# Kernel optimization log

Measured on AMD Instinct MI355X. Metric: run time of the kernel, lower is better.

The kernel has to match this reference:

```python
import jax, jax.numpy as jnp
import numpy as np
from jax import lax

B, V, ENC = 64, 2048, 128   # batch, total_voxels, encoder_dim
T = 100                      # max caption length
EMB, DEC, ATT, VOCAB = 256, 512, 256, 29


def setup_inputs() -> dict:
    key = jax.random.key(0)
    ks = jax.random.split(key, 24)
    u = lambda k, shape, s=0.1: jax.random.uniform(k, shape, jnp.float32, -s, s)
    inp = {}
    inp['encoder_output'] = jax.random.normal(ks[0], (B, V, ENC), jnp.float32)
    inp['captions'] = jax.random.randint(ks[1], (B, T), 0, VOCAB)
    # lengths sorted descending (torch loop assumes this); max length == T
    lens = jnp.sort(jax.random.randint(ks[2], (B,), 1, T + 1))[::-1]
    inp['caption_lengths'] = lens.at[0].set(T)
    # parameters (torch Linear: y = x @ W.T + b; kaiming-ish uniform)
    inp['emb_W'] = u(ks[3], (VOCAB, EMB))                       # embed init uniform(-0.1,0.1)
    inp['W_enc'] = u(ks[4], (ATT, ENC), ENC ** -0.5)
    inp['b_enc'] = u(ks[5], (ATT,), ENC ** -0.5)
    inp['W_dec'] = u(ks[6], (ATT, DEC), DEC ** -0.5)
    inp['b_dec'] = u(ks[7], (ATT,), DEC ** -0.5)
    inp['w_full'] = u(ks[8], (ATT,), ATT ** -0.5)               # full_att weight [1,ATT] -> vector
    inp['b_full'] = u(ks[9], (), ATT ** -0.5)
    lstm_in = EMB + ENC
    inp['W_ih'] = u(ks[10], (4 * DEC, lstm_in), DEC ** -0.5)
    inp['b_ih'] = u(ks[11], (4 * DEC,), DEC ** -0.5)
    inp['W_hh'] = u(ks[12], (4 * DEC, DEC), DEC ** -0.5)
    inp['b_hh'] = u(ks[13], (4 * DEC,), DEC ** -0.5)
    inp['W_init_h'] = u(ks[14], (DEC, ENC), ENC ** -0.5)
    inp['b_init_h'] = u(ks[15], (DEC,), ENC ** -0.5)
    inp['W_init_c'] = u(ks[16], (DEC, ENC), ENC ** -0.5)
    inp['b_init_c'] = u(ks[17], (DEC,), ENC ** -0.5)
    inp['W_beta'] = u(ks[18], (ENC, DEC), DEC ** -0.5)
    inp['b_beta'] = u(ks[19], (ENC,), DEC ** -0.5)
    inp['W_final'] = u(ks[20], (VOCAB, DEC))                    # uniform(-0.1,0.1) per init_weights
    inp['b_final'] = jnp.zeros((VOCAB,), jnp.float32)
    return inp


def reference(encoder_output, captions, caption_lengths, emb_W,
              W_enc, b_enc, W_dec, b_dec, w_full, b_full,
              W_ih, b_ih, W_hh, b_hh,
              W_init_h, b_init_h, W_init_c, b_init_c,
              W_beta, b_beta, W_final, b_final):
    # dropout in eval mode (identity) for deterministic reference
    emb = emb_W[captions]                                  # [B,T,EMB]
    enc_att = encoder_output @ W_enc.T + b_enc             # [B,V,ATT] (loop-invariant)
    mean_enc = encoder_output.mean(axis=1)                 # [B,ENC]
    h0 = mean_enc @ W_init_h.T + b_init_h                  # [B,DEC]
    c0 = mean_enc @ W_init_c.T + b_init_c
    lengths = caption_lengths

    def step(carry, xs):
        h, c = carry
        emb_t, t = xs                                      # [B,EMB], scalar
        # additive attention
        dec_att = h @ W_dec.T + b_dec                      # [B,ATT]
        scores = jax.nn.relu(enc_att + dec_att[:, None, :]) @ w_full + b_full  # [B,V]
        alpha = jax.nn.softmax(scores, axis=1)
        awe = jnp.einsum('bv,bve->be', alpha, encoder_output)                   # [B,ENC]
        gate = jax.nn.sigmoid(h @ W_beta.T + b_beta)
        awe = gate * awe
        # LSTMCell (torch gate order: i, f, g, o)
        x = jnp.concatenate([emb_t, awe], axis=1)          # [B,EMB+ENC]
        gates = x @ W_ih.T + b_ih + h @ W_hh.T + b_hh      # [B,4*DEC]
        i, f, g, o = jnp.split(gates, 4, axis=1)
        i, f, o = jax.nn.sigmoid(i), jax.nn.sigmoid(f), jax.nn.sigmoid(o)
        g = jnp.tanh(g)
        c_new = f * c + i * g
        h_new = o * jnp.tanh(c_new)
        pred = h_new @ W_final.T + b_final                 # [B,VOCAB]
        # length-based truncation: only rows with t < length are updated
        m = (t < lengths)[:, None]
        h2 = jnp.where(m, h_new, h)
        c2 = jnp.where(m, c_new, c)
        pred = jnp.where(m, pred, 0.0)
        alpha = jnp.where(m, alpha, 0.0)
        return (h2, c2), (pred, alpha)

    (_, _), (preds, alphas) = lax.scan(
        step, (h0, c0), (emb.transpose(1, 0, 2), jnp.arange(T)))
    predictions = preds.transpose(1, 0, 2)                 # [B,T,VOCAB]
    alphas = alphas.transpose(1, 0, 2)                     # [B,T,V]
    return predictions, alphas, caption_lengths
```

## Files before the change

kernel.cpp:

```cpp
#include <hip/hip_runtime.h>
#include <hip/hip_bf16.h>

#define BB 64
#define VV 2048
#define ENCD 128
#define TT 100
#define EMBD 256
#define DECD 512
#define ATTD 256
#define NVOCAB 29

typedef unsigned int u32;
typedef unsigned short u16;
typedef __attribute__((ext_vector_type(2))) float f2;

__device__ __forceinline__ float sigf(float x) { return 1.0f / (1.0f + __expf(-x)); }
__device__ __forceinline__ u16 to_bf16(float f) {
    u32 u = __float_as_uint(f);
    u += 0x7fffu + ((u >> 16) & 1u);
    return (u16)(u >> 16);
}

#if __has_builtin(__builtin_amdgcn_cvt_pk_fp8_f32) && __has_builtin(__builtin_amdgcn_cvt_pk_f32_fp8)
#define HAVE_FP8_CVT 1
#endif

__device__ __forceinline__ u32 fp8_enc(float f) {
#ifdef HAVE_FP8_CVT
    return (u32)__builtin_amdgcn_cvt_pk_fp8_f32(f, f, 0, false) & 0xffu;
#else
    u32 u = __float_as_uint(f);
    u32 s = (u >> 24) & 0x80u;
    u32 a = u & 0x7fffffffu;
    u32 r = a + 0x7FFFFu + ((a >> 20) & 1u);
    int v = (int)(r >> 20) - (120 << 3);
    if (v < 8) v = 0;
    if (v > 0x7E) v = 0x7E;
    return s | (u32)v;
#endif
}
__device__ __forceinline__ void fp8x4_dec(u32 u, float* o) {
#ifdef HAVE_FP8_CVT
    f2 lo = __builtin_amdgcn_cvt_pk_f32_fp8((int)u, false);
    f2 hi = __builtin_amdgcn_cvt_pk_f32_fp8((int)u, true);
    o[0] = lo[0]; o[1] = lo[1]; o[2] = hi[0]; o[3] = hi[1];
#else
    #pragma unroll
    for (int i = 0; i < 4; i++) {
        u32 byte = (u >> (8 * i)) & 0xffu;
        u32 s = (byte & 0x80u) << 24;
        u32 m = byte & 0x7fu;
        o[i] = m ? __uint_as_float(s | ((m + (120u << 3)) << 20)) : __uint_as_float(s);
    }
#endif
}


__global__ __launch_bounds__(256) void k_transpose(const float* __restrict__ W_dec,
                                                   const float* __restrict__ W_beta,
                                                   const float* __restrict__ W_ih,
                                                   const float* __restrict__ W_enc,
                                                   float* __restrict__ W_decT,
                                                   float* __restrict__ W_betaT,
                                                   float* __restrict__ W2T,
                                                   float* __restrict__ W_encT) {
    int i = blockIdx.x * 256 + threadIdx.x;
    if (i < DECD * ATTD) {
        int l = i / ATTD, a = i % ATTD;
        W_decT[i] = W_dec[a * DECD + l];
    } else if (i < DECD * ATTD + DECD * ENCD) {
        int j = i - DECD * ATTD;
        int l = j / ENCD, e = j % ENCD;
        W_betaT[j] = W_beta[e * DECD + l];
    } else if (i < DECD * ATTD + DECD * ENCD + ENCD * 2048) {
        int j = i - (DECD * ATTD + DECD * ENCD);
        int e = j >> 11, g = j & 2047;
        W2T[j] = W_ih[g * 384 + 256 + e];
    } else if (i < DECD * ATTD + DECD * ENCD + ENCD * 2048 + ENCD * ATTD) {
        int j = i - (DECD * ATTD + DECD * ENCD + ENCD * 2048);
        int k = j / ATTD, a = j % ATTD;
        W_encT[j] = W_enc[a * ENCD + k];
    }
}

__global__ __launch_bounds__(256) void k_enc_att(const float* __restrict__ enc,
                                                 const float* __restrict__ W_encT,
                                                 const float* __restrict__ b_enc,
                                                 unsigned char* __restrict__ enc_att8,
                                                 u16* __restrict__ enc_bf) {
    __shared__ float tile[64][ENCD + 1];
    int b = blockIdx.y, v0 = blockIdx.x * 64;
    int t = threadIdx.x;
    const float* src = enc + ((size_t)b * VV + v0) * ENCD;
    u16* dstb = enc_bf + ((size_t)b * VV + v0) * ENCD;
    for (int i = t; i < 64 * ENCD; i += 256) {
        float x = src[i];
        tile[i >> 7][i & 127] = x;
        dstb[i] = to_bf16(x);
    }
    __syncthreads();
    int vl = t & 63;
    int ag = __builtin_amdgcn_readfirstlane(t >> 6);
    int q = v0 >> 10, vin = (v0 & 1023) + vl;
    unsigned char* dst8 = enc_att8 + (((size_t)(b * 2 + q) * 256) << 10) + vin;
    for (int ao = 0; ao < 8; ao++) {
        int a0 = ag * 64 + ao * 8;
        float acc[8];
        #pragma unroll
        for (int j = 0; j < 8; j++) acc[j] = b_enc[a0 + j];
        const float* wT = W_encT + a0;
        #pragma unroll 4
        for (int k = 0; k < ENCD; k++) {
            float x = tile[vl][k];
            #pragma unroll
            for (int j = 0; j < 8; j++) acc[j] = fmaf(x, wT[k * ATTD + j], acc[j]);
        }
        #pragma unroll
        for (int j = 0; j < 8; j++)
            dst8[(size_t)(a0 + j) << 10] = (unsigned char)fp8_enc(acc[j]);
    }
}

__global__ __launch_bounds__(512) void k_init(const float* __restrict__ enc,
                                              const int* __restrict__ lens,
                                              const int* __restrict__ captions,
                                              const float* __restrict__ emb_W,
                                              const float* __restrict__ W_init_h,
                                              const float* __restrict__ b_init_h,
                                              const float* __restrict__ W_init_c,
                                              const float* __restrict__ b_init_c,
                                              const float* __restrict__ W_decT,
                                              const float* __restrict__ b_dec,
                                              const float* __restrict__ W_betaT,
                                              const float* __restrict__ b_beta,
                                              float* __restrict__ c0,
                                              float* __restrict__ xT,
                                              float* __restrict__ dec_att,
                                              float* __restrict__ gate0,
                                              float* __restrict__ out_len) {
    __shared__ float part[512];
    __shared__ float mean[ENCD];
    __shared__ float h_s[DECD];
    int b = blockIdx.x, t = threadIdx.x;
    int e = t & 127, ch = t >> 7;
    float s = 0.f;
    const float* rowb = enc + (size_t)b * VV * ENCD;
    for (int v = ch * 512; v < ch * 512 + 512; v++) s += rowb[(size_t)v * ENCD + e];
    part[t] = s;
    __syncthreads();
    if (ch == 0) mean[e] = (part[e] + part[128 + e] + part[256 + e] + part[384 + e]) * (1.0f / VV);
    __syncthreads();
    {
        int d = t;
        float hh = b_init_h[d], cc = b_init_c[d];
        for (int k = 0; k < ENCD; k++) {
            hh = fmaf(mean[k], W_init_h[d * ENCD + k], hh);
            cc = fmaf(mean[k], W_init_c[d * ENCD + k], cc);
        }
        c0[b * DECD + d] = cc;
        h_s[d] = hh;
        xT[(384 + d) * BB + b] = hh;
    }
    __syncthreads();
    if (t < ATTD) {
        float s2 = b_dec[t];
        for (int l = 0; l < DECD; l++) s2 = fmaf(h_s[l], W_decT[l * ATTD + t], s2);
        dec_att[b * ATTD + t] = s2;
    } else if (t < ATTD + ENCD) {
        int ee = t - ATTD;
        float s2 = b_beta[ee];
        for (int l = 0; l < DECD; l++) s2 = fmaf(h_s[l], W_betaT[l * ENCD + ee], s2);
        gate0[b * ENCD + ee] = sigf(s2);
    } else {
        int k = t - 384;
        int cap = captions[b * TT + 0];
        xT[k * BB + b] = emb_W[cap * EMBD + k];
        xT[(k + 128) * BB + b] = emb_W[cap * EMBD + k + 128];
    }
    if (t == 0) out_len[b] = (float)lens[b];
}


__global__ __launch_bounds__(256) void k_att(const unsigned char* __restrict__ enc_att8,
                                             const u16* __restrict__ enc_bf,
                                             const float* __restrict__ dec_att,
                                             const float* __restrict__ w_full,
                                             const int* __restrict__ lens,
                                             const float* __restrict__ xT,
                                             const float* __restrict__ W_ih,
                                             const float* __restrict__ W_hh,
                                             const float* __restrict__ b_ih,
                                             const float* __restrict__ b_hh,
                                             u16* __restrict__ escoreT,
                                             float* __restrict__ dpartT,
                                             float* __restrict__ pawe,
                                             float* __restrict__ gates_part, int ts) {
    int blk = blockIdx.x, t = threadIdx.x;
    int lane = t & 63, wv = t >> 6;
    if (blk < 128) {
        int b = blk >> 1, q = blk & 1;
        if (ts >= lens[b]) return;
        __shared__ float sp[4][1024];
        __shared__ float esh[1024];
        __shared__ float dred[4];
        __shared__ float redw[4][ENCD];
        {
            const uint4* sp4 = (const uint4*)((const u32*)enc_att8 +
                               (((size_t)(b * 2 + q)) << 16)) + lane;
            const float* db = dec_att + b * ATTD + wv * 64;
            const float* wf = w_full + wv * 64;
            float acc[16];
            #pragma unroll
            for (int j = 0; j < 16; j++) acc[j] = 0.f;
            #pragma unroll 16
            for (int i = 0; i < 64; i++) {
                uint4 u = sp4[(size_t)(wv * 64 + i) * 64];
                float x[16];
                fp8x4_dec(u.x, x);
                fp8x4_dec(u.y, x + 4);
                fp8x4_dec(u.z, x + 8);
                fp8x4_dec(u.w, x + 12);
                float da = db[i], wfv = wf[i];
                #pragma unroll
                for (int j = 0; j < 16; j++)
                    acc[j] = fmaf(fmaxf(x[j] + da, 0.f), wfv, acc[j]);
            }
            #pragma unroll
            for (int j = 0; j < 4; j++)
                *(float4*)&sp[wv][16 * lane + 4 * j] =
                    make_float4(acc[4 * j], acc[4 * j + 1], acc[4 * j + 2], acc[4 * j + 3]);
        }
        __syncthreads();
        float sv[4];
        #pragma unroll
        for (int j = 0; j < 4; j++)
            sv[j] = ((sp[0][4 * t + j] + sp[1][4 * t + j]) + sp[2][4 * t + j]) + sp[3][4 * t + j];
        float e0 = __expf(sv[0]), e1 = __expf(sv[1]), e2 = __expf(sv[2]), e3 = __expf(sv[3]);
        uint2 pk;
        pk.x = (u32)to_bf16(e0) | ((u32)to_bf16(e1) << 16);
        pk.y = (u32)to_bf16(e2) | ((u32)to_bf16(e3) << 16);
        ((uint2*)escoreT)[(((size_t)ts * BB + b) * VV + (q << 10)) / 4 + t] = pk;
        esh[4 * t] = e0; esh[4 * t + 1] = e1; esh[4 * t + 2] = e2; esh[4 * t + 3] = e3;
        float ss = e0 + e1 + e2 + e3;
        for (int o = 32; o > 0; o >>= 1) ss += __shfl_down(ss, o);
        if (lane == 0) dred[wv] = ss;
        __syncthreads();
        if (t == 0) dpartT[((size_t)ts * BB + b) * 2 + q] =
                        dred[0] + dred[1] + dred[2] + dred[3];
        const u32* eb = (const u32*)enc_bf + ((size_t)b * VV + (q << 10)) * (ENCD / 2) + lane;
        float a0 = 0.f, a1 = 0.f;
        #pragma unroll 32
        for (int vv = wv; vv < 1024; vv += 4) {
            u32 u = eb[(size_t)vv * 64];
            float sc = esh[vv];
            a0 = fmaf(__uint_as_float(u << 16), sc, a0);
            a1 = fmaf(__uint_as_float(u & 0xffff0000u), sc, a1);
        }
        redw[wv][2 * lane] = a0;
        redw[wv][2 * lane + 1] = a1;
        __syncthreads();
        if (t < ENCD)
            pawe[((size_t)b * 2 + q) * ENCD + t] =
                redw[0][t] + redw[1][t] + redw[2][t] + redw[3][t];
    } else {
        int idx = blk - 128;
        int kcp = idx >> 6;
        int kc = kcp < 2 ? kcp : kcp + 1;
        int gt = idx & 63;
        int gbase = gt * 32 + wv * 8;
        int gb = __builtin_amdgcn_readfirstlane(gbase);
        int k0 = kc * 128;
        float acc[8];
        #pragma unroll
        for (int j = 0; j < 8; j++)
            acc[j] = (kc == 0) ? (b_ih[gb + j] + b_hh[gb + j]) : 0.f;
        if (kc < 2) {
            #pragma unroll 16
            for (int kk = 0; kk < 128; kk++) {
                float xv = xT[(k0 + kk) * BB + lane];
                #pragma unroll
                for (int j = 0; j < 8; j++)
                    acc[j] = fmaf(xv, W_ih[(gb + j) * 384 + k0 + kk], acc[j]);
            }
        } else {
            const float* Wh = W_hh + (k0 - 384);
            #pragma unroll 16
            for (int kk = 0; kk < 128; kk++) {
                float xv = xT[(k0 + kk) * BB + lane];
                #pragma unroll
                for (int j = 0; j < 8; j++)
                    acc[j] = fmaf(xv, Wh[(gb + j) * DECD + kk], acc[j]);
            }
        }
        float4* o4 = (float4*)(gates_part + ((size_t)kcp * BB + lane) * 2048 + gbase);
        o4[0] = make_float4(acc[0], acc[1], acc[2], acc[3]);
        o4[1] = make_float4(acc[4], acc[5], acc[6], acc[7]);
    }
}

__global__ __launch_bounds__(512) void k_cell(const float* __restrict__ gates_part,
                                              const float* __restrict__ dpartT,
                                              const float* __restrict__ pawe,
                                              const int* __restrict__ lens,
                                              const int* __restrict__ captions,
                                              const float* __restrict__ emb_W,
                                              const float* __restrict__ W2T,
                                              const float* __restrict__ W_final,
                                              const float* __restrict__ b_final,
                                              const float* __restrict__ W_decT,
                                              const float* __restrict__ b_dec,
                                              const float* __restrict__ W_betaT,
                                              const float* __restrict__ b_beta,
                                              float* __restrict__ gate0,
                                              float* __restrict__ gate1,
                                              float* __restrict__ c0,
                                              float* __restrict__ c1,
                                              float* __restrict__ xT,
                                              float* __restrict__ dec_att,
                                              float* __restrict__ preds, int ts) {
    int b = blockIdx.x >> 2, part = blockIdx.x & 3;
    if (ts >= lens[b]) return;
    __shared__ float gawe_s[ENCD];
    __shared__ float h_s[DECD];
    __shared__ float red[512];
    int t = threadIdx.x;
    const float* dp = dpartT + ((size_t)ts * BB + b) * 2;
    float inv = 1.0f / (dp[0] + dp[1]);
    const float* gprev = (ts & 1) ? gate1 : gate0;
    float*       gnext = (ts & 1) ? gate0 : gate1;
    if (t < ENCD) {
        const float* pw = pawe + (size_t)b * 2 * ENCD + t;
        float aw = (pw[0] + pw[ENCD]) * inv;
        gawe_s[t] = gprev[b * ENCD + t] * aw;
    }
    __syncthreads();
    const float* cin  = (ts & 1) ? c1 : c0;
    float*       cout = (ts & 1) ? c0 : c1;
    {
        float gi = 0.f, gf = 0.f, gg = 0.f, go = 0.f;
        #pragma unroll
        for (int sc = 0; sc < 6; sc++) {
            const float* gp = gates_part + ((size_t)sc * BB + b) * 2048;
            gi += gp[t]; gf += gp[512 + t]; gg += gp[1024 + t]; go += gp[1536 + t];
        }
        #pragma unroll 16
        for (int e = 0; e < ENCD; e++) {
            const float* w = W2T + (size_t)e * 2048;
            float ge = gawe_s[e];
            gi = fmaf(w[t], ge, gi);
            gf = fmaf(w[512 + t], ge, gf);
            gg = fmaf(w[1024 + t], ge, gg);
            go = fmaf(w[1536 + t], ge, go);
        }
        gi = sigf(gi); gf = sigf(gf); go = sigf(go); gg = tanhf(gg);
        float cn = fmaf(gf, cin[b * DECD + t], gi * gg);
        float hn = go * tanhf(cn);
        h_s[t] = hn;
        if (part == 0) {
            cout[b * DECD + t] = cn;
            xT[(384 + t) * BB + b] = hn;
        }
    }
    __syncthreads();
    if (part < 2) {
        int a = (t & 127) + part * 128, qq = t >> 7;
        float s = 0.f;
        const float* wd = W_decT + (size_t)qq * 128 * ATTD + a;
        #pragma unroll 16
        for (int l = 0; l < 128; l++) s = fmaf(h_s[qq * 128 + l], wd[(size_t)l * ATTD], s);
        red[t] = s;
        __syncthreads();
        if (t < 128)
            dec_att[b * ATTD + t + part * 128] =
                red[t] + red[t + 128] + red[t + 256] + red[t + 384] + b_dec[t + part * 128];
    } else if (part == 2) {
        int e = t & 127, qq = t >> 7;
        float s = 0.f;
        const float* wb = W_betaT + (size_t)qq * 128 * ENCD + e;
        #pragma unroll 16
        for (int l = 0; l < 128; l++) s = fmaf(h_s[qq * 128 + l], wb[(size_t)l * ENCD], s);
        red[t] = s;
        __syncthreads();
        if (t < 128)
            gnext[b * ENCD + t] = sigf(red[t] + red[t + 128] + red[t + 256] + red[t + 384]
                                       + b_beta[t]);
    } else {
        int lane = t & 63, wv = t >> 6;
        for (int j = wv; j < NVOCAB; j += 8) {
            float s2 = 0.f;
            #pragma unroll
            for (int i = 0; i < 8; i++)
                s2 = fmaf(h_s[lane + 64 * i], W_final[j * DECD + lane + 64 * i], s2);
            for (int o = 32; o > 0; o >>= 1) s2 += __shfl_down(s2, o);
            if (lane == 0) preds[((size_t)b * TT + ts) * NVOCAB + j] = s2 + b_final[j];
        }
        if (t < 256 && ts + 1 < TT) {
            int cap = captions[b * TT + ts + 1];
            xT[t * BB + b] = emb_W[cap * EMBD + t];
        }
    }
}

__global__ __launch_bounds__(256) void k_alphas(const u16* __restrict__ escoreT,
                                                const float* __restrict__ dpartT,
                                                const int* __restrict__ lens,
                                                float* __restrict__ alphas) {
    int ts = blockIdx.x, b = blockIdx.y, t = threadIdx.x;
    if (ts >= lens[b]) return;
    const float* dp = dpartT + ((size_t)ts * BB + b) * 2;
    float inv = 1.0f / (dp[0] + dp[1]);
    const u32* es = (const u32*)escoreT + ((size_t)ts * BB + b) * VV / 2;
    float2* al = (float2*)(alphas + ((size_t)b * TT + ts) * VV);
    #pragma unroll
    for (int i = t; i < VV / 2; i += 256) {
        u32 u = es[i];
        al[i] = make_float2(__uint_as_float(u << 16) * inv,
                            __uint_as_float(u & 0xffff0000u) * inv);
    }
}

extern "C" void kernel_launch(void* const* d_in, const int* in_sizes, int n_in,
                              void* d_out, int out_size, void* d_ws, size_t ws_size,
                              hipStream_t stream) {
    const float* enc      = (const float*)d_in[0];
    const int*   captions = (const int*)d_in[1];
    const int*   lens     = (const int*)d_in[2];
    const float* emb_W    = (const float*)d_in[3];
    const float* W_enc    = (const float*)d_in[4];
    const float* b_enc    = (const float*)d_in[5];
    const float* W_dec    = (const float*)d_in[6];
    const float* b_dec    = (const float*)d_in[7];
    const float* w_full   = (const float*)d_in[8];
    const float* W_ih     = (const float*)d_in[10];
    const float* b_ih     = (const float*)d_in[11];
    const float* W_hh     = (const float*)d_in[12];
    const float* b_hh     = (const float*)d_in[13];
    const float* W_init_h = (const float*)d_in[14];
    const float* b_init_h = (const float*)d_in[15];
    const float* W_init_c = (const float*)d_in[16];
    const float* b_init_c = (const float*)d_in[17];
    const float* W_beta   = (const float*)d_in[18];
    const float* b_beta   = (const float*)d_in[19];
    const float* W_final  = (const float*)d_in[20];
    const float* b_final  = (const float*)d_in[21];

    float* preds   = (float*)d_out;
    float* alphas  = preds + (size_t)BB * TT * NVOCAB;
    float* out_len = alphas + (size_t)BB * TT * VV;

    char* ws = (char*)d_ws;
    size_t off = 0;
    auto alloc = [&](size_t bytes) {
        char* p = ws + off;
        off += (bytes + 255) & ~(size_t)255;
        return p;
    };
    unsigned char* enc_att8 = (unsigned char*)alloc((size_t)BB * ATTD * VV);
    u16*   enc_bf     = (u16*)  alloc((size_t)BB * VV * ENCD * sizeof(u16));
    u16*   escoreT    = (u16*)  alloc((size_t)TT * BB * VV * sizeof(u16));
    float* dpartT     = (float*)alloc((size_t)TT * BB * 2 * sizeof(float));
    float* pawe       = (float*)alloc((size_t)BB * 2 * ENCD * sizeof(float));
    float* dec_att    = (float*)alloc((size_t)BB * ATTD * sizeof(float));
    float* gate0      = (float*)alloc((size_t)BB * ENCD * sizeof(float));
    float* gate1      = (float*)alloc((size_t)BB * ENCD * sizeof(float));
    float* xT         = (float*)alloc((size_t)896 * BB * sizeof(float));
    float* gates_part = (float*)alloc((size_t)6 * BB * 2048 * sizeof(float));
    float* c0         = (float*)alloc((size_t)BB * DECD * sizeof(float));
    float* c1         = (float*)alloc((size_t)BB * DECD * sizeof(float));
    float* W_decT     = (float*)alloc((size_t)DECD * ATTD * sizeof(float));
    float* W_betaT    = (float*)alloc((size_t)DECD * ENCD * sizeof(float));
    float* W2T        = (float*)alloc((size_t)ENCD * 2048 * sizeof(float));
    float* W_encT     = (float*)alloc((size_t)ENCD * ATTD * sizeof(float));

    hipMemsetAsync(d_out, 0, (size_t)out_size * sizeof(float), stream);

    k_transpose<<<1920, 256, 0, stream>>>(W_dec, W_beta, W_ih, W_enc,
                                          W_decT, W_betaT, W2T, W_encT);
    k_enc_att<<<dim3(VV / 64, BB), 256, 0, stream>>>(enc, W_encT, b_enc, enc_att8, enc_bf);
    k_init<<<BB, 512, 0, stream>>>(enc, lens, captions, emb_W, W_init_h, b_init_h,
                                   W_init_c, b_init_c, W_decT, b_dec, W_betaT, b_beta,
                                   c0, xT, dec_att, gate0, out_len);

    for (int t = 0; t < TT; t++) {
        k_att<<<512, 256, 0, stream>>>(enc_att8, enc_bf, dec_att, w_full, lens, xT,
                                       W_ih, W_hh, b_ih, b_hh, escoreT, dpartT, pawe,
                                       gates_part, t);
        k_cell<<<256, 512, 0, stream>>>(gates_part, dpartT, pawe, lens, captions, emb_W,
                                        W2T, W_final, b_final, W_decT, b_dec, W_betaT,
                                        b_beta, gate0, gate1, c0, c1, xT, dec_att,
                                        preds, t);
    }
    k_alphas<<<dim3(TT, BB), 256, 0, stream>>>(escoreT, dpartT, lens, alphas);
}
```

Before: 4.977 ms.

## Move gated attention-weighted-encoding projection into attention kernel

The W_ih projection of the gated attention-weighted encoding moves out of the cell kernel and into the attention blocks. Each (batch, half) block now applies the beta gate to its partial sum and multiplies by W2T, writing two extra gates_part slices. The cell kernel sums those slices and scales by the softmax normaliser, since the projection is linear. This removes the serial 128-step matvec from the cell kernel's critical path and spreads it over 128 blocks, but each attention block does extra work and the partial-gate buffer traffic grows. The encoder-attention inner loop unroll is also raised.

```diff
diff --git a/kernel.cpp b/kernel.cpp
--- a/kernel.cpp
+++ b/kernel.cpp
@@ -109,7 +109,7 @@
         #pragma unroll
         for (int j = 0; j < 8; j++) acc[j] = b_enc[a0 + j];
         const float* wT = W_encT + a0;
-        #pragma unroll 4
+        #pragma unroll 8
         for (int k = 0; k < ENCD; k++) {
             float x = tile[vl][k];
             #pragma unroll
@@ -191,9 +191,11 @@
                                              const float* __restrict__ W_hh,
                                              const float* __restrict__ b_ih,
                                              const float* __restrict__ b_hh,
+                                             const float* __restrict__ W2T,
+                                             const float* __restrict__ gate0,
+                                             const float* __restrict__ gate1,
                                              u16* __restrict__ escoreT,
                                              float* __restrict__ dpartT,
-                                             float* __restrict__ pawe,
                                              float* __restrict__ gates_part, int ts) {
     int blk = blockIdx.x, t = threadIdx.x;
     int lane = t & 63, wv = t >> 6;
@@ -204,6 +206,7 @@
         __shared__ float esh[1024];
         __shared__ float dred[4];
         __shared__ float redw[4][ENCD];
+        __shared__ float gawe_s[ENCD];
         {
             const uint4* sp4 = (const uint4*)((const u32*)enc_att8 +
                                (((size_t)(b * 2 + q)) << 16)) + lane;
@@ -259,9 +262,27 @@
         redw[wv][2 * lane] = a0;
         redw[wv][2 * lane + 1] = a1;
         __syncthreads();
-        if (t < ENCD)
-            pawe[((size_t)b * 2 + q) * ENCD + t] =
-                redw[0][t] + redw[1][t] + redw[2][t] + redw[3][t];
+        if (t < ENCD) {
+            const float* gprev = (ts & 1) ? gate1 : gate0;
+            gawe_s[t] = (redw[0][t] + redw[1][t] + redw[2][t] + redw[3][t])
+                        * gprev[b * ENCD + t];
+        }
+        __syncthreads();
+        {
+            float acc[8];
+            #pragma unroll
+            for (int j = 0; j < 8; j++) acc[j] = 0.f;
+            #pragma unroll 8
+            for (int e = 0; e < ENCD; e++) {
+                const float* w = W2T + (size_t)e * 2048 + 8 * t;
+                float ge = gawe_s[e];
+                #pragma unroll
+                for (int j = 0; j < 8; j++) acc[j] = fmaf(w[j], ge, acc[j]);
+            }
+            float4* o4 = (float4*)(gates_part + ((size_t)(6 + q) * BB + b) * 2048 + 8 * t);
+            o4[0] = make_float4(acc[0], acc[1], acc[2], acc[3]);
+            o4[1] = make_float4(acc[4], acc[5], acc[6], acc[7]);
+        }
     } else {
         int idx = blk - 128;
         int kcp = idx >> 6;
@@ -300,11 +321,9 @@
 
 __global__ __launch_bounds__(512) void k_cell(const float* __restrict__ gates_part,
                                               const float* __restrict__ dpartT,
-                                              const float* __restrict__ pawe,
                                               const int* __restrict__ lens,
                                               const int* __restrict__ captions,
                                               const float* __restrict__ emb_W,
-                                              const float* __restrict__ W2T,
                                               const float* __restrict__ W_final,
                                               const float* __restrict__ b_final,
                                               const float* __restrict__ W_decT,
@@ -320,20 +339,12 @@
                                               float* __restrict__ preds, int ts) {
     int b = blockIdx.x >> 2, part = blockIdx.x & 3;
     if (ts >= lens[b]) return;
-    __shared__ float gawe_s[ENCD];
     __shared__ float h_s[DECD];
     __shared__ float red[512];
     int t = threadIdx.x;
     const float* dp = dpartT + ((size_t)ts * BB + b) * 2;
     float inv = 1.0f / (dp[0] + dp[1]);
-    const float* gprev = (ts & 1) ? gate1 : gate0;
-    float*       gnext = (ts & 1) ? gate0 : gate1;
-    if (t < ENCD) {
-        const float* pw = pawe + (size_t)b * 2 * ENCD + t;
-        float aw = (pw[0] + pw[ENCD]) * inv;
-        gawe_s[t] = gprev[b * ENCD + t] * aw;
-    }
-    __syncthreads();
+    float* gnext = (ts & 1) ? gate0 : gate1;
     const float* cin  = (ts & 1) ? c1 : c0;
     float*       cout = (ts & 1) ? c0 : c1;
     {
@@ -343,15 +354,12 @@
             const float* gp = gates_part + ((size_t)sc * BB + b) * 2048;
             gi += gp[t]; gf += gp[512 + t]; gg += gp[1024 + t]; go += gp[1536 + t];
         }
-        #pragma unroll 16
-        for (int e = 0; e < ENCD; e++) {
-            const float* w = W2T + (size_t)e * 2048;
-            float ge = gawe_s[e];
-            gi = fmaf(w[t], ge, gi);
-            gf = fmaf(w[512 + t], ge, gf);
-            gg = fmaf(w[1024 + t], ge, gg);
-            go = fmaf(w[1536 + t], ge, go);
-        }
+        const float* g6 = gates_part + ((size_t)6 * BB + b) * 2048;
+        const float* g7 = gates_part + ((size_t)7 * BB + b) * 2048;
+        gi += (g6[t] + g7[t]) * inv;
+        gf += (g6[512 + t] + g7[512 + t]) * inv;
+        gg += (g6[1024 + t] + g7[1024 + t]) * inv;
+        go += (g6[1536 + t] + g7[1536 + t]) * inv;
         gi = sigf(gi); gf = sigf(gf); go = sigf(go); gg = tanhf(gg);
         float cn = fmaf(gf, cin[b * DECD + t], gi * gg);
         float hn = go * tanhf(cn);
@@ -459,12 +467,11 @@
     u16*   enc_bf     = (u16*)  alloc((size_t)BB * VV * ENCD * sizeof(u16));
     u16*   escoreT    = (u16*)  alloc((size_t)TT * BB * VV * sizeof(u16));
     float* dpartT     = (float*)alloc((size_t)TT * BB * 2 * sizeof(float));
-    float* pawe       = (float*)alloc((size_t)BB * 2 * ENCD * sizeof(float));
     float* dec_att    = (float*)alloc((size_t)BB * ATTD * sizeof(float));
     float* gate0      = (float*)alloc((size_t)BB * ENCD * sizeof(float));
     float* gate1      = (float*)alloc((size_t)BB * ENCD * sizeof(float));
     float* xT         = (float*)alloc((size_t)896 * BB * sizeof(float));
-    float* gates_part = (float*)alloc((size_t)6 * BB * 2048 * sizeof(float));
+    float* gates_part = (float*)alloc((size_t)8 * BB * 2048 * sizeof(float));
     float* c0         = (float*)alloc((size_t)BB * DECD * sizeof(float));
     float* c1         = (float*)alloc((size_t)BB * DECD * sizeof(float));
     float* W_decT     = (float*)alloc((size_t)DECD * ATTD * sizeof(float));
@@ -483,10 +490,10 @@
 
     for (int t = 0; t < TT; t++) {
         k_att<<<512, 256, 0, stream>>>(enc_att8, enc_bf, dec_att, w_full, lens, xT,
-                                       W_ih, W_hh, b_ih, b_hh, escoreT, dpartT, pawe,
-                                       gates_part, t);
-        k_cell<<<256, 512, 0, stream>>>(gates_part, dpartT, pawe, lens, captions, emb_W,
-                                        W2T, W_final, b_final, W_decT, b_dec, W_betaT,
+                                       W_ih, W_hh, b_ih, b_hh, W2T, gate0, gate1,
+                                       escoreT, dpartT, gates_part, t);
+        k_cell<<<256, 512, 0, stream>>>(gates_part, dpartT, lens, captions, emb_W,
+                                        W_final, b_final, W_decT, b_dec, W_betaT,
                                         b_beta, gate0, gate1, c0, c1, xT, dec_att,
                                         preds, t);
     }
```

Result: slower. 5.077 ms (+2.0%).
